# Performance work log

Measured on AMD Instinct MI355X. Metric: run time of the kernel, lower is better.

The kernel has to match this reference:

```python
import jax, jax.numpy as jnp
import numpy as np

WINDOW = 7
NUM_HEADS = 16
HEAD_DIM = 32  # dim 512 / 16 heads
SCALE = HEAD_DIM ** -0.5


def _relative_position_index(ws: int) -> np.ndarray:
    coords = np.stack(np.meshgrid(np.arange(ws), np.arange(ws), indexing='ij'))  # [2, ws, ws]
    flat = coords.reshape(2, -1)  # [2, N]
    rel = flat[:, :, None] - flat[:, None, :]  # [2, N, N]
    rel = rel.transpose(1, 2, 0)  # [N, N, 2]
    rh = (rel[:, :, 0] + ws - 1) * (2 * ws - 1)
    rw = rel[:, :, 1] + ws - 1
    return (rh + rw).astype(np.int32)  # [N, N]

REL_IDX = jnp.asarray(_relative_position_index(WINDOW))  # [49, 49]


def setup_inputs() -> dict:
    key = jax.random.key(0)
    ks = jax.random.split(key, 4)
    B, N, C = 4096, WINDOW * WINDOW, 512
    x = jax.random.normal(ks[0], (B, N, C), dtype=jnp.float32)
    qkv_w = jax.random.normal(ks[1], (C, 3 * C), dtype=jnp.float32) * (C ** -0.5)
    qkv_b = jnp.zeros((3 * C,), dtype=jnp.float32)
    proj_w = jax.random.normal(ks[2], (C, C), dtype=jnp.float32) * (C ** -0.5)
    proj_b = jnp.zeros((C,), dtype=jnp.float32)
    bias_table = jax.random.normal(ks[3], ((2 * WINDOW - 1) ** 2, NUM_HEADS), dtype=jnp.float32) * 0.02
    return {"x": x, "qkv_w": qkv_w, "qkv_b": qkv_b, "proj_w": proj_w,
            "proj_b": proj_b, "bias_table": bias_table}


def reference(x, qkv_w, qkv_b, proj_w, proj_b, bias_table):
    B, N, C = x.shape
    # QKV projection -> [B, N, 3, H, D] -> q/k/v [B, H, N, D]
    qkv = (x @ qkv_w + qkv_b).reshape(B, N, 3, NUM_HEADS, HEAD_DIM)
    qkv = jnp.transpose(qkv, (2, 0, 3, 1, 4))
    q, k, v = qkv[0], qkv[1], qkv[2]
    attn = jnp.einsum('bhnd,bhmd->bhnm', q * SCALE, k)  # [B, H, N, N]
    # relative position bias gather: [N*N, H] -> [1, H, N, N]
    bias = bias_table[REL_IDX.reshape(-1)].reshape(N, N, NUM_HEADS)
    attn = attn + jnp.transpose(bias, (2, 0, 1))[None]
    attn = jax.nn.softmax(attn, axis=-1)
    out = jnp.einsum('bhnm,bhmd->bhnd', attn, v)  # [B, H, N, D]
    out = jnp.transpose(out, (0, 2, 1, 3)).reshape(B, N, C)
    return out @ proj_w + proj_b
```

## Files before the change

kernel.cpp:

```cpp
#include <hip/hip_runtime.h>

typedef _Float16 h16;
typedef __attribute__((ext_vector_type(4))) _Float16 h16x4;
typedef __attribute__((ext_vector_type(8))) _Float16 h16x8;
typedef __attribute__((ext_vector_type(4))) float f32x4;

#define QSCALE 0.25505653882616254f
#define LOG2E  1.4426950408889634f
#define MFMA16(a, b, c) __builtin_amdgcn_mfma_f32_16x16x16f16(a, b, c, 0, 0, 0)
#define MFMA32(a, b, c) __builtin_amdgcn_mfma_f32_16x16x32_f16(a, b, c, 0, 0, 0)

#define O_BYTES 205520896ULL
#define W1F_OFF (O_BYTES)
#define W2F_OFF (W1F_OFF + 1572864ULL)
#define BF_OFF  (W2F_OFF + 524288ULL)

__global__ __launch_bounds__(256) void wa_prep(
    const float* __restrict__ qkv_w, const float* __restrict__ proj_w,
    const float* __restrict__ table,
    h16* __restrict__ w1F, h16* __restrict__ w2F, float* __restrict__ biasF) {
  const int b = blockIdx.x, tid = threadIdx.x;
  if (b < 128) {
    int chunk = b * 256 + tid;
    int lane = chunk & 63;
    int rest = chunk >> 6;
    int fr = rest & 7, kt = (rest >> 3) & 7, cw = rest >> 6;
    int nt = fr >> 1, kh = fr & 1;
    int l15 = lane & 15, lg = lane >> 4;
    int o = cw * 64 + nt * 16 + l15;
    int k0 = kt * 64 + (kh * 4 + lg) * 8;
    h16x8 v;
    #pragma unroll
    for (int e = 0; e < 8; ++e)
      v[e] = (h16)proj_w[(size_t)(k0 + e) * 512 + o];
    *(h16x8*)(w2F + (size_t)chunk * 8) = v;
  } else if (b < 512) {
    int chunk = (b - 128) * 256 + tid;
    int lane = chunk & 63;
    int rest = chunk >> 6;
    int f  = rest % 12;
    int kt = (rest / 12) & 7;
    int wv = (rest / 96) & 3;
    int g  = rest / 384;
    int s = f >> 2, d = (f >> 1) & 1, ks = f & 1;
    int l15 = lane & 15, lg = lane >> 4;
    int o = s * 512 + g * 128 + wv * 32 + d * 16 + l15;
    int k0 = kt * 64 + ks * 32 + lg * 8;
    float sc = (s == 0) ? QSCALE : 1.0f;
    h16x8 v;
    #pragma unroll
    for (int e = 0; e < 8; ++e)
      v[e] = (h16)(qkv_w[(size_t)(k0 + e) * 1536 + o] * sc);
    *(h16x8*)(w1F + (size_t)chunk * 8) = v;
  } else {
    int t = (b - 512) * 256 + tid;
    int lane = t & 63, jt = (t >> 6) & 3, qt = (t >> 8) & 3, head = t >> 10;
    int l15 = lane & 15, lg = lane >> 4;
    int q = qt * 16 + l15;
    float4 v;
    #pragma unroll
    for (int r = 0; r < 4; ++r) {
      int j = jt * 16 + lg * 4 + r;
      float val = -1e30f;
      if (j < 49 && q < 49) {
        int rel = (q / 7 - j / 7 + 6) * 13 + (q % 7 - j % 7 + 6);
        val = table[rel * 16 + head] * LOG2E;
      }
      ((float*)&v)[r] = val;
    }
    ((float4*)biasF)[t] = v;
  }
}

__global__ __launch_bounds__(256, 3) void wa_qkv_attn(
    const float* __restrict__ x, const float* __restrict__ qkv_b,
    const h16* __restrict__ w1F, const float* __restrict__ biasF,
    h16* __restrict__ O) {
  __shared__ __align__(16) char lds[50176];
  const int tid = threadIdx.x;
  const int wave = tid >> 6, lane = tid & 63;
  const int l15 = lane & 15, lg = lane >> 4;
  const int sw = l15 & 7;
  const int lbid = (blockIdx.x & 7) * 1024 + (blockIdx.x >> 3);
  const int w = lbid >> 1, gp = lbid & 1;
  const size_t rowbase = (size_t)w * 49;

  #pragma unroll
  for (int p = 0; p < 13; ++p) {
    int idx = tid + p * 256;
    if (idx < 3136) {
      int r = idx >> 6, c = idx & 63;
      const float* src = x + (rowbase + r) * 512 + c * 8;
      float4 a = *(const float4*)(src);
      float4 bb = *(const float4*)(src + 4);
      h16x8 h = { (h16)a.x, (h16)a.y, (h16)a.z, (h16)a.w,
                  (h16)bb.x, (h16)bb.y, (h16)bb.z, (h16)bb.w };
      *(h16x8*)(lds + r * 1024 + ((c ^ (r & 7)) << 4)) = h;
    }
  }
  __syncthreads();

  int xbA[4], xbB[4];
  #pragma unroll
  for (int t = 0; t < 4; ++t) {
    int row = (t < 3) ? (16 * t + l15) : 48;
    int swt = (t < 3) ? sw : 0;
    xbA[t] = row * 1024 + ((lg ^ swt) << 4);
    xbB[t] = row * 1024 + (((4 + lg) ^ swt) << 4);
  }
  const h16x4 ones = (h16x4){(h16)1.f, (h16)1.f, (h16)1.f, (h16)1.f};
  const float4* bF4 = (const float4*)biasF;

#define WLOAD8(DST, KT) {                                                  \
    _Pragma("unroll") for (int f8 = 0; f8 < 8; ++f8)                       \
      DST[f8] = *(const h16x8*)(wb + (size_t)(KT) * 6144 + f8 * 512); }

#define WLOAD4V(DST, KT) {                                                 \
    _Pragma("unroll") for (int f4 = 0; f4 < 4; ++f4)                       \
      DST[f4] = *(const h16x8*)(wb + (size_t)(KT) * 6144 + (8 + f4) * 512); }

#define STEP_QK(KT, W) {                                                   \
    h16x8 xf[4];                                                           \
    _Pragma("unroll") for (int t = 0; t < 4; ++t)                          \
      xf[t] = *(const h16x8*)(lds + xbA[t] + (KT) * 128);                  \
    __builtin_amdgcn_s_setprio(1);                                         \
    _Pragma("unroll") for (int d = 0; d < 2; ++d)                          \
    _Pragma("unroll") for (int t = 0; t < 4; ++t) {                        \
      accQ[d][t] = MFMA32(W[d*2],     xf[t], accQ[d][t]);                  \
      accK[d][t] = MFMA32(W[4 + d*2], xf[t], accK[d][t]);                  \
    }                                                                      \
    __builtin_amdgcn_s_setprio(0);                                         \
    _Pragma("unroll") for (int t = 0; t < 4; ++t)                          \
      xf[t] = *(const h16x8*)(lds + xbB[t] + (KT) * 128);                  \
    __builtin_amdgcn_s_setprio(1);                                         \
    _Pragma("unroll") for (int d = 0; d < 2; ++d)                          \
    _Pragma("unroll") for (int t = 0; t < 4; ++t) {                        \
      accQ[d][t] = MFMA32(W[d*2 + 1],     xf[t], accQ[d][t]);              \
      accK[d][t] = MFMA32(W[4 + d*2 + 1], xf[t], accK[d][t]);              \
    }                                                                      \
    __builtin_amdgcn_s_setprio(0); }

#define STEP_V(KT, W) {                                                    \
    h16x8 xf[4];                                                           \
    _Pragma("unroll") for (int t = 0; t < 4; ++t)                          \
      xf[t] = *(const h16x8*)(lds + xbA[t] + (KT) * 128);                  \
    __builtin_amdgcn_s_setprio(1);                                         \
    _Pragma("unroll") for (int d = 0; d < 2; ++d)                          \
    _Pragma("unroll") for (int t = 0; t < 4; ++t)                          \
      accV[t][d] = MFMA32(xf[t], W[d*2], accV[t][d]);                      \
    __builtin_amdgcn_s_setprio(0);                                         \
    _Pragma("unroll") for (int t = 0; t < 4; ++t)                          \
      xf[t] = *(const h16x8*)(lds + xbB[t] + (KT) * 128);                  \
    __builtin_amdgcn_s_setprio(1);                                         \
    _Pragma("unroll") for (int d = 0; d < 2; ++d)                          \
    _Pragma("unroll") for (int t = 0; t < 4; ++t)                          \
      accV[t][d] = MFMA32(xf[t], W[d*2 + 1], accV[t][d]);                  \
    __builtin_amdgcn_s_setprio(0); }

#define PROCESS_HEAD(G) {                                                  \
    const int head = (G) * 4 + wave;                                       \
    const h16* wb = w1F + ((size_t)((G) * 4 + wave) * 8) * 6144 + lane * 8;\
    h16x4 Qh[2][4], Kh[2][4], Vh[4][2];                                    \
     {\
      f32x4 accQ[2][4], accK[2][4];                                        \
      _Pragma("unroll") for (int d = 0; d < 2; ++d) {                      \
        f32x4 iq, ik;                                                      \
        _Pragma("unroll") for (int r = 0; r < 4; ++r) {                    \
          iq[r] = qkv_b[head * 32 + 16 * d + 4 * lg + r] * QSCALE;         \
          ik[r] = qkv_b[512 + head * 32 + 16 * d + 4 * lg + r];            \
        }                                                                  \
        _Pragma("unroll") for (int t = 0; t < 4; ++t) {                    \
          accQ[d][t] = iq;                                                 \
          accK[d][t] = ik;                                                 \
        }                                                                  \
      }                                                                    \
      _Pragma("unroll 1") for (int kt = 0; kt < 8; ++kt) {                 \
        h16x8 WQK[8];                                                      \
        WLOAD8(WQK, kt);                                                   \
        STEP_QK(kt, WQK);                                                  \
      }                                                                    \
      _Pragma("unroll") for (int d = 0; d < 2; ++d)                        \
      _Pragma("unroll") for (int t = 0; t < 4; ++t)                        \
      _Pragma("unroll") for (int r = 0; r < 4; ++r) {                      \
        Qh[d][t][r] = (h16)accQ[d][t][r];                                  \
        Kh[d][t][r] = (h16)accK[d][t][r];                                  \
      }                                                                    \
    }                                                                      \
     {     \
      f32x4 accV[4][2];                                                    \
      _Pragma("unroll") for (int d = 0; d < 2; ++d) {                      \
        float bv = qkv_b[1024 + head * 32 + 16 * d + l15];                 \
        f32x4 iv = { bv, bv, bv, bv };                                     \
        _Pragma("unroll") for (int t = 0; t < 4; ++t) accV[t][d] = iv;     \
      }                                                                    \
      _Pragma("unroll 1") for (int kt = 0; kt < 8; ++kt) {                 \
        h16x8 WV[4];                                                       \
        WLOAD4V(WV, kt);                                                   \
        STEP_V(kt, WV);                                                    \
      }                                                                    \
      _Pragma("unroll") for (int t = 0; t < 4; ++t)                        \
      _Pragma("unroll") for (int d = 0; d < 2; ++d)                        \
      _Pragma("unroll") for (int r = 0; r < 4; ++r)                        \
        Vh[t][d][r] = (h16)accV[t][d][r];                                  \
    }                                                                      \
                   \
    f32x4 st[4][4];                                                        \
    __builtin_amdgcn_s_setprio(1);                                         \
    _Pragma("unroll") for (int jt = 0; jt < 4; ++jt)                       \
    _Pragma("unroll") for (int qt = 0; qt < 4; ++qt) {                     \
      float4 bvv = bF4[(head * 16 + qt * 4 + jt) * 64 + lane];             \
      f32x4 c0 = { bvv.x, bvv.y, bvv.z, bvv.w };                           \
      st[jt][qt] = MFMA16(Kh[0][jt], Qh[0][qt], c0);                       \
      st[jt][qt] = MFMA16(Kh[1][jt], Qh[1][qt], st[jt][qt]);               \
    }                                                                      \
    __builtin_amdgcn_s_setprio(0);                                         \
    h16x4 pf[4][4];                                                        \
    _Pragma("unroll") for (int qt = 0; qt < 4; ++qt)                       \
    _Pragma("unroll") for (int jt = 0; jt < 4; ++jt) {                     \
      h16x4 p;                                                             \
      _Pragma("unroll") for (int r = 0; r < 4; ++r)                        \
        p[r] = (h16)exp2f(st[jt][qt][r]);                                  \
      pf[jt][qt] = p;                                                      \
    }                                                                      \
    f32x4 ss[4];                                                           \
    _Pragma("unroll") for (int qt = 0; qt < 4; ++qt)                       \
      ss[qt] = (f32x4){0.f, 0.f, 0.f, 0.f};                                \
    f32x4 ot[2][4];                                                        \
    _Pragma("unroll") for (int d = 0; d < 2; ++d)                          \
    _Pragma("unroll") for (int qt = 0; qt < 4; ++qt)                       \
      ot[d][qt] = (f32x4){0.f, 0.f, 0.f, 0.f};                             \
    __builtin_amdgcn_s_setprio(1);                                         \
    _Pragma("unroll") for (int jt = 0; jt < 4; ++jt)                       \
    _Pragma("unroll") for (int qt = 0; qt < 4; ++qt) {                     \
      ss[qt] = MFMA16(ones, pf[jt][qt], ss[qt]);                           \
      _Pragma("unroll") for (int d = 0; d < 2; ++d)                        \
        ot[d][qt] = MFMA16(Vh[jt][d], pf[jt][qt], ot[d][qt]);              \
    }                                                                      \
    __builtin_amdgcn_s_setprio(0);                                         \
    _Pragma("unroll") for (int qt = 0; qt < 4; ++qt) {                     \
      int q = 16 * qt + l15;                                               \
      float ri = __builtin_amdgcn_rcpf(ss[qt][0]);                         \
      if (q < 49) {                                                        \
        h16* gdst = O + (rowbase + q) * 512 + head * 32 + 4 * lg;          \
        _Pragma("unroll") for (int d = 0; d < 2; ++d) {                    \
          h16x4 ov;                                                        \
          _Pragma("unroll") for (int r = 0; r < 4; ++r)                    \
            ov[r] = (h16)(ot[d][qt][r] * ri);                              \
          *(h16x4*)(gdst + 16 * d) = ov;                                   \
        }                                                                  \
      }                                                                    \
    } }

  PROCESS_HEAD(gp * 2);
  PROCESS_HEAD(gp * 2 + 1);
#undef PROCESS_HEAD
#undef STEP_QK
#undef STEP_V
#undef WLOAD8
#undef WLOAD4V
}

__global__ __launch_bounds__(256, 3) void wa_proj(
    const h16* __restrict__ O, const h16* __restrict__ w2F,
    const float* __restrict__ proj_b, float* __restrict__ out) {
  __shared__ __align__(16) char lds[16384];
  const int tid = threadIdx.x;
  const int wave = tid >> 6, lane = tid & 63;
  const int l15 = lane & 15, lg = lane >> 4;
  const int lbid = (blockIdx.x & 7) * 784 + (blockIdx.x >> 3);
  const int rowt = lbid >> 2, colt = lbid & 3;
  const int wr = wave >> 1, wc = wave & 1;
  const h16* wb2 = w2F + (size_t)(colt * 2 + wc) * 32768 + lane * 8;

  f32x4 acc[4][4];
  #pragma unroll
  for (int a = 0; a < 4; ++a)
    #pragma unroll
    for (int b = 0; b < 4; ++b) acc[a][b] = (f32x4){0.f, 0.f, 0.f, 0.f};

  h16x8 pre[4];
  #pragma unroll
  for (int p = 0; p < 4; ++p) {
    int idx = tid + p * 256;
    int r = idx >> 3, c = idx & 7;
    pre[p] = *(const h16x8*)(O + (size_t)(rowt * 128 + r) * 512 + c * 8);
  }
  #pragma unroll
  for (int p = 0; p < 4; ++p) {
    int idx = tid + p * 256;
    int r = idx >> 3, c = idx & 7;
    *(h16x8*)(lds + r * 128 + ((c ^ (r & 7)) << 4)) = pre[p];
  }
  __syncthreads();

  for (int kt = 0; kt < 8; ++kt) {
    if (kt < 7) {
      #pragma unroll
      for (int p = 0; p < 4; ++p) {
        int idx = tid + p * 256;
        int r = idx >> 3, c = idx & 7;
        pre[p] = *(const h16x8*)(O + (size_t)(rowt * 128 + r) * 512 + (kt + 1) * 64 + c * 8);
      }
    }
    #pragma unroll
    for (int kh = 0; kh < 2; ++kh) {
      const int sw = (l15 & 7);
      h16x8 af[4], bf[4];
      #pragma unroll
      for (int mt = 0; mt < 4; ++mt) {
        int r = wr * 64 + 16 * mt + l15;
        af[mt] = *(const h16x8*)(lds + r * 128 + (((kh * 4 + lg) ^ sw) << 4));
      }
      #pragma unroll
      for (int nt = 0; nt < 4; ++nt)
        bf[nt] = *(const h16x8*)(wb2 + (size_t)(kt * 8 + nt * 2 + kh) * 512);
      __builtin_amdgcn_s_setprio(1);
      #pragma unroll
      for (int mt = 0; mt < 4; ++mt)
        #pragma unroll
        for (int nt = 0; nt < 4; ++nt)
          acc[mt][nt] = MFMA32(af[mt], bf[nt], acc[mt][nt]);
      __builtin_amdgcn_s_setprio(0);
    }
    __syncthreads();
    if (kt < 7) {
      #pragma unroll
      for (int p = 0; p < 4; ++p) {
        int idx = tid + p * 256;
        int r = idx >> 3, c = idx & 7;
        *(h16x8*)(lds + r * 128 + ((c ^ (r & 7)) << 4)) = pre[p];
      }
      __syncthreads();
    }
  }
  #pragma unroll
  for (int nt = 0; nt < 4; ++nt) {
    int col = colt * 128 + wc * 64 + nt * 16 + l15;
    float pb = proj_b[col];
    #pragma unroll
    for (int mt = 0; mt < 4; ++mt) {
      int row = rowt * 128 + wr * 64 + mt * 16 + 4 * lg;
      #pragma unroll
      for (int r = 0; r < 4; ++r)
        out[(size_t)(row + r) * 512 + col] = acc[mt][nt][r] + pb;
    }
  }
}

extern "C" void kernel_launch(void* const* d_in, const int* in_sizes, int n_in,
                              void* d_out, int out_size, void* d_ws, size_t ws_size,
                              hipStream_t stream) {
  const float* x          = (const float*)d_in[0];
  const float* qkv_w      = (const float*)d_in[1];
  const float* qkv_b      = (const float*)d_in[2];
  const float* proj_w     = (const float*)d_in[3];
  const float* proj_b     = (const float*)d_in[4];
  const float* bias_table = (const float*)d_in[5];
  float* out = (float*)d_out;

  char* ws = (char*)d_ws;
  h16*   O     = (h16*)ws;
  h16*   w1F   = (h16*)(ws + W1F_OFF);
  h16*   w2F   = (h16*)(ws + W2F_OFF);
  float* biasF = (float*)(ws + BF_OFF);

  wa_prep<<<576, 256, 0, stream>>>(qkv_w, proj_w, bias_table, w1F, w2F, biasF);
  wa_qkv_attn<<<8192, 256, 0, stream>>>(x, qkv_b, w1F, biasF, O);
  wa_proj<<<1568 * 4, 256, 0, stream>>>(O, w2F, proj_b, out);
}
```

Before: 696.2 us.

## Process all heads of a window in one block to avoid reloading x

```diff
diff --git a/kernel.cpp b/kernel.cpp
--- a/kernel.cpp
+++ b/kernel.cpp
@@ -81,8 +81,7 @@
   const int wave = tid >> 6, lane = tid & 63;
   const int l15 = lane & 15, lg = lane >> 4;
   const int sw = l15 & 7;
-  const int lbid = (blockIdx.x & 7) * 1024 + (blockIdx.x >> 3);
-  const int w = lbid >> 1, gp = lbid & 1;
+  const int w = (blockIdx.x & 7) * 512 + (blockIdx.x >> 3);
   const size_t rowbase = (size_t)w * 49;
 
   #pragma unroll
@@ -157,103 +156,130 @@
       accV[t][d] = MFMA32(xf[t], W[d*2 + 1], accV[t][d]);                  \
     __builtin_amdgcn_s_setprio(0); }
 
-#define PROCESS_HEAD(G) {                                                  \
-    const int head = (G) * 4 + wave;                                       \
-    const h16* wb = w1F + ((size_t)((G) * 4 + wave) * 8) * 6144 + lane * 8;\
-    h16x4 Qh[2][4], Kh[2][4], Vh[4][2];                                    \
-     {\
-      f32x4 accQ[2][4], accK[2][4];                                        \
-      _Pragma("unroll") for (int d = 0; d < 2; ++d) {                      \
-        f32x4 iq, ik;                                                      \
-        _Pragma("unroll") for (int r = 0; r < 4; ++r) {                    \
-          iq[r] = qkv_b[head * 32 + 16 * d + 4 * lg + r] * QSCALE;         \
-          ik[r] = qkv_b[512 + head * 32 + 16 * d + 4 * lg + r];            \
-        }                                                                  \
-        _Pragma("unroll") for (int t = 0; t < 4; ++t) {                    \
-          accQ[d][t] = iq;                                                 \
-          accK[d][t] = ik;                                                 \
-        }                                                                  \
-      }                                                                    \
-      _Pragma("unroll 1") for (int kt = 0; kt < 8; ++kt) {                 \
-        h16x8 WQK[8];                                                      \
-        WLOAD8(WQK, kt);                                                   \
-        STEP_QK(kt, WQK);                                                  \
-      }                                                                    \
-      _Pragma("unroll") for (int d = 0; d < 2; ++d)                        \
-      _Pragma("unroll") for (int t = 0; t < 4; ++t)                        \
-      _Pragma("unroll") for (int r = 0; r < 4; ++r) {                      \
-        Qh[d][t][r] = (h16)accQ[d][t][r];                                  \
-        Kh[d][t][r] = (h16)accK[d][t][r];                                  \
-      }                                                                    \
-    }                                                                      \
-     {     \
-      f32x4 accV[4][2];                                                    \
-      _Pragma("unroll") for (int d = 0; d < 2; ++d) {                      \
-        float bv = qkv_b[1024 + head * 32 + 16 * d + l15];                 \
-        f32x4 iv = { bv, bv, bv, bv };                                     \
-        _Pragma("unroll") for (int t = 0; t < 4; ++t) accV[t][d] = iv;     \
-      }                                                                    \
-      _Pragma("unroll 1") for (int kt = 0; kt < 8; ++kt) {                 \
-        h16x8 WV[4];                                                       \
-        WLOAD4V(WV, kt);                                                   \
-        STEP_V(kt, WV);                                                    \
-      }                                                                    \
-      _Pragma("unroll") for (int t = 0; t < 4; ++t)                        \
-      _Pragma("unroll") for (int d = 0; d < 2; ++d)                        \
-      _Pragma("unroll") for (int r = 0; r < 4; ++r)                        \
-        Vh[t][d][r] = (h16)accV[t][d][r];                                  \
-    }                                                                      \
-                   \
-    f32x4 st[4][4];                                                        \
-    __builtin_amdgcn_s_setprio(1);                                         \
-    _Pragma("unroll") for (int jt = 0; jt < 4; ++jt)                       \
-    _Pragma("unroll") for (int qt = 0; qt < 4; ++qt) {                     \
-      float4 bvv = bF4[(head * 16 + qt * 4 + jt) * 64 + lane];             \
-      f32x4 c0 = { bvv.x, bvv.y, bvv.z, bvv.w };                           \
-      st[jt][qt] = MFMA16(Kh[0][jt], Qh[0][qt], c0);                       \
-      st[jt][qt] = MFMA16(Kh[1][jt], Qh[1][qt], st[jt][qt]);               \
-    }                                                                      \
-    __builtin_amdgcn_s_setprio(0);                                         \
-    h16x4 pf[4][4];                                                        \
-    _Pragma("unroll") for (int qt = 0; qt < 4; ++qt)                       \
-    _Pragma("unroll") for (int jt = 0; jt < 4; ++jt) {                     \
-      h16x4 p;                                                             \
-      _Pragma("unroll") for (int r = 0; r < 4; ++r)                        \
-        p[r] = (h16)exp2f(st[jt][qt][r]);                                  \
-      pf[jt][qt] = p;                                                      \
-    }                                                                      \
-    f32x4 ss[4];                                                           \
-    _Pragma("unroll") for (int qt = 0; qt < 4; ++qt)                       \
-      ss[qt] = (f32x4){0.f, 0.f, 0.f, 0.f};                                \
-    f32x4 ot[2][4];                                                        \
-    _Pragma("unroll") for (int d = 0; d < 2; ++d)                          \
-    _Pragma("unroll") for (int qt = 0; qt < 4; ++qt)                       \
-      ot[d][qt] = (f32x4){0.f, 0.f, 0.f, 0.f};                             \
-    __builtin_amdgcn_s_setprio(1);                                         \
-    _Pragma("unroll") for (int jt = 0; jt < 4; ++jt)                       \
-    _Pragma("unroll") for (int qt = 0; qt < 4; ++qt) {                     \
-      ss[qt] = MFMA16(ones, pf[jt][qt], ss[qt]);                           \
-      _Pragma("unroll") for (int d = 0; d < 2; ++d)                        \
-        ot[d][qt] = MFMA16(Vh[jt][d], pf[jt][qt], ot[d][qt]);              \
-    }                                                                      \
-    __builtin_amdgcn_s_setprio(0);                                         \
-    _Pragma("unroll") for (int qt = 0; qt < 4; ++qt) {                     \
-      int q = 16 * qt + l15;                                               \
-      float ri = __builtin_amdgcn_rcpf(ss[qt][0]);                         \
-      if (q < 49) {                                                        \
-        h16* gdst = O + (rowbase + q) * 512 + head * 32 + 4 * lg;          \
-        _Pragma("unroll") for (int d = 0; d < 2; ++d) {                    \
-          h16x4 ov;                                                        \
-          _Pragma("unroll") for (int r = 0; r < 4; ++r)                    \
-            ov[r] = (h16)(ot[d][qt][r] * ri);                              \
-          *(h16x4*)(gdst + 16 * d) = ov;                                   \
-        }                                                                  \
-      }                                                                    \
-    } }
-
-  PROCESS_HEAD(gp * 2);
-  PROCESS_HEAD(gp * 2 + 1);
-#undef PROCESS_HEAD
+  #pragma unroll 1
+  for (int g = 0; g < 4; ++g) {
+    const int head = g * 4 + wave;
+    const h16* wb = w1F + ((size_t)(g * 4 + wave) * 8) * 6144 + lane * 8;
+    h16x4 Qh[2][4], Kh[2][4], Vh[4][2];
+
+    {
+      f32x4 accQ[2][4], accK[2][4];
+      #pragma unroll
+      for (int d = 0; d < 2; ++d) {
+        f32x4 iq, ik;
+        #pragma unroll
+        for (int r = 0; r < 4; ++r) {
+          iq[r] = qkv_b[head * 32 + 16 * d + 4 * lg + r] * QSCALE;
+          ik[r] = qkv_b[512 + head * 32 + 16 * d + 4 * lg + r];
+        }
+        #pragma unroll
+        for (int t = 0; t < 4; ++t) {
+          accQ[d][t] = iq;
+          accK[d][t] = ik;
+        }
+      }
+      #pragma unroll 1
+      for (int kt = 0; kt < 8; ++kt) {
+        h16x8 WQK[8];
+        WLOAD8(WQK, kt);
+        STEP_QK(kt, WQK);
+      }
+      #pragma unroll
+      for (int d = 0; d < 2; ++d)
+        #pragma unroll
+        for (int t = 0; t < 4; ++t)
+          #pragma unroll
+          for (int r = 0; r < 4; ++r) {
+            Qh[d][t][r] = (h16)accQ[d][t][r];
+            Kh[d][t][r] = (h16)accK[d][t][r];
+          }
+    }
+
+    {
+      f32x4 accV[4][2];
+      #pragma unroll
+      for (int d = 0; d < 2; ++d) {
+        float bv = qkv_b[1024 + head * 32 + 16 * d + l15];
+        f32x4 iv = { bv, bv, bv, bv };
+        #pragma unroll
+        for (int t = 0; t < 4; ++t) accV[t][d] = iv;
+      }
+      #pragma unroll 1
+      for (int kt = 0; kt < 8; ++kt) {
+        h16x8 WV[4];
+        WLOAD4V(WV, kt);
+        STEP_V(kt, WV);
+      }
+      #pragma unroll
+      for (int t = 0; t < 4; ++t)
+        #pragma unroll
+        for (int d = 0; d < 2; ++d)
+          #pragma unroll
+          for (int r = 0; r < 4; ++r)
+            Vh[t][d][r] = (h16)accV[t][d][r];
+    }
+
+    f32x4 st[4][4];
+    __builtin_amdgcn_s_setprio(1);
+    #pragma unroll
+    for (int jt = 0; jt < 4; ++jt)
+      #pragma unroll
+      for (int qt = 0; qt < 4; ++qt) {
+        float4 bvv = bF4[(head * 16 + qt * 4 + jt) * 64 + lane];
+        f32x4 c0 = { bvv.x, bvv.y, bvv.z, bvv.w };
+        st[jt][qt] = MFMA16(Kh[0][jt], Qh[0][qt], c0);
+        st[jt][qt] = MFMA16(Kh[1][jt], Qh[1][qt], st[jt][qt]);
+      }
+    __builtin_amdgcn_s_setprio(0);
+
+    h16x4 pf[4][4];
+    #pragma unroll
+    for (int qt = 0; qt < 4; ++qt)
+      #pragma unroll
+      for (int jt = 0; jt < 4; ++jt) {
+        h16x4 p;
+        #pragma unroll
+        for (int r = 0; r < 4; ++r)
+          p[r] = (h16)exp2f(st[jt][qt][r]);
+        pf[jt][qt] = p;
+      }
+
+    f32x4 ss[4];
+    #pragma unroll
+    for (int qt = 0; qt < 4; ++qt) ss[qt] = (f32x4){0.f, 0.f, 0.f, 0.f};
+    f32x4 ot[2][4];
+    #pragma unroll
+    for (int d = 0; d < 2; ++d)
+      #pragma unroll
+      for (int qt = 0; qt < 4; ++qt) ot[d][qt] = (f32x4){0.f, 0.f, 0.f, 0.f};
+    __builtin_amdgcn_s_setprio(1);
+    #pragma unroll
+    for (int jt = 0; jt < 4; ++jt)
+      #pragma unroll
+      for (int qt = 0; qt < 4; ++qt) {
+        ss[qt] = MFMA16(ones, pf[jt][qt], ss[qt]);
+        #pragma unroll
+        for (int d = 0; d < 2; ++d)
+          ot[d][qt] = MFMA16(Vh[jt][d], pf[jt][qt], ot[d][qt]);
+      }
+    __builtin_amdgcn_s_setprio(0);
+
+    #pragma unroll
+    for (int qt = 0; qt < 4; ++qt) {
+      int q = 16 * qt + l15;
+      float ri = __builtin_amdgcn_rcpf(ss[qt][0]);
+      if (q < 49) {
+        h16* gdst = O + (rowbase + q) * 512 + head * 32 + 4 * lg;
+        #pragma unroll
+        for (int d = 0; d < 2; ++d) {
+          h16x4 ov;
+          #pragma unroll
+          for (int r = 0; r < 4; ++r) ov[r] = (h16)(ot[d][qt][r] * ri);
+          *(h16x4*)(gdst + 16 * d) = ov;
+        }
+      }
+    }
+  }
 #undef STEP_QK
 #undef STEP_V
 #undef WLOAD8
@@ -365,6 +391,6 @@
   float* biasF = (float*)(ws + BF_OFF);
 
   wa_prep<<<576, 256, 0, stream>>>(qkv_w, proj_w, bias_table, w1F, w2F, biasF);
-  wa_qkv_attn<<<8192, 256, 0, stream>>>(x, qkv_b, w1F, biasF, O);
+  wa_qkv_attn<<<4096, 256, 0, stream>>>(x, qkv_b, w1F, biasF, O);
   wa_proj<<<1568 * 4, 256, 0, stream>>>(O, w2F, proj_b, out);
 }
```

Result: no change. 685.4 us (-1.5%).
